# Optimization experiments

Hardware: AMD Instinct MI355X
Metric: run time of the kernel (lower is better)

Reference implementation:

```python
import jax, jax.numpy as jnp
import numpy as np

N = 50000      # nodes
E = 800000     # edges (avg degree 16)
IN = 128       # input feature dim
H = 128        # hidden dim (all layers output H; out_channels unused in source)
DROP_P = 0.5


def setup_inputs() -> dict:
    key = jax.random.key(0)
    ks = jax.random.split(key, 8)
    s_in = 1.0 / np.sqrt(IN).astype(np.float32)
    s_h = 1.0 / np.sqrt(H).astype(np.float32)
    return {
        "x": jax.random.normal(ks[0], (N, IN), jnp.float32),
        "edge_index": jax.random.randint(ks[1], (2, E), 0, N, dtype=jnp.int32),
        "Wl0": jax.random.normal(ks[2], (H, IN), jnp.float32) * s_in,
        "bl0": jnp.zeros((H,), jnp.float32),
        "Wr0": jax.random.normal(ks[3], (H, IN), jnp.float32) * s_in,
        "Wl1": jax.random.normal(ks[4], (H, H), jnp.float32) * s_h,
        "bl1": jnp.zeros((H,), jnp.float32),
        "Wr1": jax.random.normal(ks[5], (H, H), jnp.float32) * s_h,
    }


def _sage_conv(x, src, dst, Wl, bl, Wr):
    # mean-aggregate neighbor messages: gather x[src], scatter-add to dst
    agg = jax.ops.segment_sum(x[src], dst, num_segments=N)          # [N, D]
    deg = jax.ops.segment_sum(jnp.ones((src.shape[0],), x.dtype), dst,
                              num_segments=N)                        # [N]
    agg = agg / jnp.maximum(deg, 1.0)[:, None]                       # scatter_mean (0 for isolated nodes)
    # PyG SAGEConv: lin_l(agg) (with bias) + lin_r(x) (no bias)
    return agg @ Wl.T + bl + x @ Wr.T


def reference(x, edge_index, Wl0, bl0, Wr0, Wl1, bl1, Wr1):
    src, dst = edge_index[0], edge_index[1]
    h = _sage_conv(x, src, dst, Wl0, bl0, Wr0)
    h = jax.nn.relu(h)
    # dropout(p=0.5, training=True) with a fixed key for determinism
    keep = jax.random.bernoulli(jax.random.key(42), 1.0 - DROP_P, h.shape)
    h = jnp.where(keep, h / (1.0 - DROP_P), 0.0)
    out = _sage_conv(h, src, dst, Wl1, bl1, Wr1)
    return out
```

## Files before the change

### kernel.cpp

```cpp
#include <hip/hip_runtime.h>
#include <hip/hip_bf16.h>


#define HDIM 128
#define KDIM 256
#define NBUK 256
#define BNODE 196
#define BCAP 4096
#define BCH 2048

typedef __attribute__((ext_vector_type(8))) short bshort8;
typedef __attribute__((ext_vector_type(4))) float f32x4;
typedef __attribute__((ext_vector_type(2))) float f32x2;

__device__ __forceinline__ ushort f2b(float f) {
  __hip_bfloat16 h = __float2bfloat16(f);
  return *(ushort*)&h;
}
__device__ __forceinline__ unsigned int pack2(float lo, float hi) {
  return (unsigned int)f2b(lo) | ((unsigned int)f2b(hi) << 16);
}

#if __has_builtin(__builtin_amdgcn_cvt_pk_f32_fp8) && __has_builtin(__builtin_amdgcn_cvt_pk_fp8_f32)
#define FP8_HW 1
#endif

__device__ __forceinline__ unsigned int fp8e1(float f) {
  unsigned int u = __float_as_uint(f);
  unsigned int s = (u >> 24) & 0x80u;
  unsigned int mag = u & 0x7FFFFFFFu;
  if (mag < 0x38800000u) return s;
  if (mag > 0x43E00000u) mag = 0x43E00000u;
  unsigned int r = mag + 0x7FFFFu + ((mag >> 20) & 1u);
  return s | ((r >> 20) - 960u);
}
__device__ __forceinline__ float fp8d1(unsigned int b) {
  unsigned int v = b & 0x7Fu;
  float fn = __uint_as_float(((b & 0x80u) << 24) | ((v + 960u) << 20));
  return v >= 8u ? fn : 0.0f;
}

__device__ __forceinline__ unsigned int fp8x4_enc(float f0, float f1, float f2, float f3) {
#ifdef FP8_HW
  int u = 0;
  u = __builtin_amdgcn_cvt_pk_fp8_f32(f0, f1, u, false);
  u = __builtin_amdgcn_cvt_pk_fp8_f32(f2, f3, u, true);
  return (unsigned int)u;
#else
  return fp8e1(f0) | (fp8e1(f1) << 8) | (fp8e1(f2) << 16) | (fp8e1(f3) << 24);
#endif
}
__device__ __forceinline__ void fp8x4_acc(float* a, unsigned int w) {
#ifdef FP8_HW
  f32x2 lo = __builtin_amdgcn_cvt_pk_f32_fp8((int)w, false);
  f32x2 hi = __builtin_amdgcn_cvt_pk_f32_fp8((int)w, true);
  a[0] += lo.x; a[1] += lo.y; a[2] += hi.x; a[3] += hi.y;
#else
  a[0] += fp8d1(w & 255u); a[1] += fp8d1((w >> 8) & 255u);
  a[2] += fp8d1((w >> 16) & 255u); a[3] += fp8d1(w >> 24);
#endif
}

__device__ __forceinline__ unsigned int tf_rotl(unsigned int x, int d) {
  return (x << d) | (x >> (32 - d));
}
__device__ __forceinline__ bool dropout_keep(unsigned int j) {
  unsigned int x0 = 0u, x1 = j;
  const unsigned int ks0 = 0u, ks1 = 42u, ks2 = 0x1BD11BDAu ^ 0u ^ 42u;
  x0 += ks0; x1 += ks1;
#define TF_R(r) { x0 += x1; x1 = tf_rotl(x1, (r)); x1 ^= x0; }
  TF_R(13) TF_R(15) TF_R(26) TF_R(6)
  x0 += ks1; x1 += ks2 + 1u;
  TF_R(17) TF_R(29) TF_R(16) TF_R(24)
  x0 += ks2; x1 += ks0 + 2u;
  TF_R(13) TF_R(15) TF_R(26) TF_R(6)
  x0 += ks0; x1 += ks1 + 3u;
  TF_R(17) TF_R(29) TF_R(16) TF_R(24)
  x0 += ks1; x1 += ks2 + 4u;
  TF_R(13) TF_R(15) TF_R(26) TF_R(6)
  x0 += ks2; x1 += ks0 + 5u;
#undef TF_R
  unsigned int r = x0 ^ x1;
  float u = __uint_as_float((r >> 9) | 0x3f800000u) - 1.0f;
  return u < 0.5f;
}

__global__ __launch_bounds__(256) void bin_cvt_k(
    const int* __restrict__ src, const int* __restrict__ dst,
    int* __restrict__ bucketCount, unsigned int* __restrict__ pairs, int E, int EB,
    const float* __restrict__ x,
    const float* __restrict__ Wl0, const float* __restrict__ Wr0,
    const float* __restrict__ Wl1, const float* __restrict__ Wr1,
    ushort* __restrict__ Xb, unsigned char* __restrict__ Xq,
    ushort* __restrict__ Wc0, ushort* __restrict__ Wc1, int N) {
  __shared__ int hist[NBUK];
  __shared__ int lofs[NBUK];
  __shared__ int lcur[NBUK];
  __shared__ int gbase[NBUK];
  __shared__ unsigned int ordv[BCH];
  __shared__ unsigned char ordb[BCH];

  int b = blockIdx.x;
  if (b >= EB) {
    b -= EB;
    if (b < 64) {
      int t = b * 256 + threadIdx.x;
      int o = t >> 7, k = t & 127;
      Wc0[o * KDIM + k] = f2b(Wl0[t]);
      Wc0[o * KDIM + HDIM + k] = f2b(Wr0[t]);
      Wc1[o * KDIM + k] = f2b(Wl1[t]);
      Wc1[o * KDIM + HDIM + k] = f2b(Wr1[t]);
    } else {
      int t = (b - 64) * 256 + threadIdx.x;
      if (t < N * 32) {
        int n = t >> 5, c4 = t & 31;
        float4 v = *(const float4*)&x[(size_t)n * HDIM + c4 * 4];
        uint2 p;
        p.x = pack2(v.x, v.y);
        p.y = pack2(v.z, v.w);
        *(uint2*)&Xb[(size_t)n * HDIM + c4 * 4] = p;
        *(unsigned int*)&Xq[(size_t)n * HDIM + c4 * 4] = fp8x4_enc(v.x, v.y, v.z, v.w);
      }
    }
    return;
  }

  hist[threadIdx.x] = 0;
  __syncthreads();
  int begin = b * BCH;
  int n = min(BCH, E - begin);
  unsigned int vals[BCH / 256];
  int bks[BCH / 256];
  int cnt = 0;
  for (int i = threadIdx.x; i < n; i += 256) {
    int s = src[begin + i], d = dst[begin + i];
    int bk = d / BNODE;
    int dloc = d - bk * BNODE;
    vals[cnt] = ((unsigned int)s << 8) | (unsigned int)dloc;
    bks[cnt] = bk;
    ++cnt;
    atomicAdd(&hist[bk], 1);
  }
  __syncthreads();
  {
    int v = hist[threadIdx.x];
    lofs[threadIdx.x] = v;
    __syncthreads();
    for (int off = 1; off < NBUK; off <<= 1) {
      int t = (threadIdx.x >= off) ? lofs[threadIdx.x - off] : 0;
      __syncthreads();
      lofs[threadIdx.x] += t;
      __syncthreads();
    }
    int ex = lofs[threadIdx.x] - v;
    __syncthreads();
    lofs[threadIdx.x] = ex;
    lcur[threadIdx.x] = ex;
    gbase[threadIdx.x] = atomicAdd(&bucketCount[threadIdx.x], v);
  }
  __syncthreads();
  for (int k = 0; k < cnt; ++k) {
    int bk = bks[k];
    int p = atomicAdd(&lcur[bk], 1);
    ordv[p] = vals[k];
    ordb[p] = (unsigned char)bk;
  }
  __syncthreads();
  for (int j = threadIdx.x; j < n; j += 256) {
    int bk = ordb[j];
    pairs[bk * BCAP + gbase[bk] + (j - lofs[bk])] = ordv[j];
  }
}

__global__ __launch_bounds__(256) void build_k(const unsigned int* __restrict__ pairs,
                                               const int* __restrict__ bucketCount,
                                               int* __restrict__ deg,
                                               int* __restrict__ rowptr,
                                               ushort* __restrict__ eidx, int N) {
  __shared__ int h[BNODE];
  __shared__ int lofs[BNODE];
  __shared__ int cur[BNODE];
  const int b = blockIdx.x;
  const int base = b * BCAP;
  const int cnt = bucketCount[b];
  const int nodebase = b * BNODE;
  const int nloc = min(BNODE, N - nodebase);
  if (threadIdx.x < BNODE) h[threadIdx.x] = 0;
  __syncthreads();
  for (int i = threadIdx.x; i < cnt; i += 256) atomicAdd(&h[pairs[base + i] & 255u], 1);
  __syncthreads();
  if (threadIdx.x < BNODE) lofs[threadIdx.x] = h[threadIdx.x];
  __syncthreads();
  for (int off = 1; off < BNODE; off <<= 1) {
    int t = (threadIdx.x >= off && threadIdx.x < BNODE) ? lofs[threadIdx.x - off] : 0;
    __syncthreads();
    if (threadIdx.x < BNODE) lofs[threadIdx.x] += t;
    __syncthreads();
  }
  if (threadIdx.x < BNODE) {
    int ex = lofs[threadIdx.x] - h[threadIdx.x];
    cur[threadIdx.x] = ex;
    if (threadIdx.x < nloc) {
      deg[nodebase + threadIdx.x] = h[threadIdx.x];
      rowptr[nodebase + threadIdx.x] = base + ex;
    }
  }
  __syncthreads();
  for (int i = threadIdx.x; i < cnt; i += 256) {
    unsigned int v = pairs[base + i];
    int pos = atomicAdd(&cur[v & 255u], 1);
    eidx[base + pos] = (ushort)(v >> 8);
  }
}

__global__ __launch_bounds__(256) void agg_q(const unsigned char* __restrict__ Fq,
                                             ushort* __restrict__ Ag,
                                             const ushort* __restrict__ eidx,
                                             const int* __restrict__ rowptr,
                                             const int* __restrict__ deg, int N) {
  const int lane = threadIdx.x & 63;
  const int n = blockIdx.x * 4 + (threadIdx.x >> 6);
  if (n >= N) return;
  const int start = rowptr[n];
  const int d = deg[n];
  const int es = lane >> 3;
  const int cl = lane & 7;
  float a[16];
#pragma unroll
  for (int i = 0; i < 16; ++i) a[i] = 0.0f;
  for (int j = 0; j < d; j += 16) {
    uint4 v[2];
    bool m[2];
#pragma unroll
    for (int u = 0; u < 2; ++u) {
      int e = j + u * 8 + es;
      m[u] = e < d;
      if (m[u]) {
        int s = eidx[start + e];
        v[u] = *(const uint4*)&Fq[(size_t)s * HDIM + cl * 16];
      }
    }
#pragma unroll
    for (int u = 0; u < 2; ++u)
      if (m[u]) {
        fp8x4_acc(&a[0], v[u].x);
        fp8x4_acc(&a[4], v[u].y);
        fp8x4_acc(&a[8], v[u].z);
        fp8x4_acc(&a[12], v[u].w);
      }
  }
#pragma unroll
  for (int i = 0; i < 16; ++i) {
    a[i] += __shfl_xor(a[i], 8, 64);
    a[i] += __shfl_xor(a[i], 16, 64);
    a[i] += __shfl_xor(a[i], 32, 64);
  }
  if (es == 0) {
    float rd = 1.0f / fmaxf((float)d, 1.0f);
    uint4 p0, p1;
    p0.x = pack2(a[0] * rd, a[1] * rd);
    p0.y = pack2(a[2] * rd, a[3] * rd);
    p0.z = pack2(a[4] * rd, a[5] * rd);
    p0.w = pack2(a[6] * rd, a[7] * rd);
    p1.x = pack2(a[8] * rd, a[9] * rd);
    p1.y = pack2(a[10] * rd, a[11] * rd);
    p1.z = pack2(a[12] * rd, a[13] * rd);
    p1.w = pack2(a[14] * rd, a[15] * rd);
    *(uint4*)&Ag[(size_t)n * HDIM + cl * 16] = p0;
    *(uint4*)&Ag[(size_t)n * HDIM + cl * 16 + 8] = p1;
  }
}

template <int MODE>
__global__ __launch_bounds__(256) void gemm_mfma(const ushort* __restrict__ Agg,
                                                 const ushort* __restrict__ F,
                                                 const ushort* __restrict__ Wc,
                                                 ushort* __restrict__ hb,
                                                 unsigned char* __restrict__ hq,
                                                 float* __restrict__ fout,
                                                 const float* __restrict__ bias,
                                                 int N) {
  __shared__ char smem[34816];
  ushort* Wl = (ushort*)smem;
  float* Tl = (float*)smem;
  const int tid = threadIdx.x;
  const int lane = tid & 63;
  const int wid = tid >> 6;
  const int quad = lane >> 4;
  const int l15 = lane & 15;
  const int n0 = blockIdx.x * 64;

  int rowA = n0 + wid * 16 + l15;
  if (rowA >= N) rowA = N - 1;
  bshort8 afA[4], afF[4];
#pragma unroll
  for (int ks = 0; ks < 4; ++ks) {
    afA[ks] = *(const bshort8*)&Agg[(size_t)rowA * HDIM + ks * 32 + quad * 8];
    afF[ks] = *(const bshort8*)&F[(size_t)rowA * HDIM + ks * 32 + quad * 8];
  }

  f32x4 acc[8];
#pragma unroll
  for (int i = 0; i < 8; ++i) acc[i] = (f32x4){0.f, 0.f, 0.f, 0.f};

#pragma unroll
  for (int half = 0; half < 2; ++half) {
    __syncthreads();
#pragma unroll
    for (int i = 0; i < 8; ++i) {
      int q = i * 256 + tid;
      int row = q >> 4, seg = q & 15;
      *(uint4*)&Wl[row * 136 + seg * 8] = *(const uint4*)&Wc[row * KDIM + half * HDIM + seg * 8];
    }
    __syncthreads();
#pragma unroll
    for (int ks = 0; ks < 4; ++ks) {
#pragma unroll
      for (int os = 0; os < 8; ++os) {
        bshort8 bf = *(const bshort8*)&Wl[(os * 16 + l15) * 136 + ks * 32 + quad * 8];
        acc[os] = __builtin_amdgcn_mfma_f32_16x16x32_bf16(
            half == 0 ? afA[ks] : afF[ks], bf, acc[os], 0, 0, 0);
      }
    }
  }

  __syncthreads();

  const int wbase = wid * (16 * 132);
#pragma unroll
  for (int os = 0; os < 8; ++os)
#pragma unroll
    for (int r = 0; r < 4; ++r)
      Tl[wbase + (quad * 4 + r) * 132 + os * 16 + l15] = acc[os][r];

  __syncthreads();

#pragma unroll
  for (int i = 0; i < 8; ++i) {
    int q = i * 64 + lane;
    int r = q >> 5;
    int c4 = q & 31;
    int n = n0 + wid * 16 + r;
    if (n >= N) continue;
    int c = c4 * 4;
    float4 v = *(float4*)&Tl[wbase + r * 132 + c];
    const float4 bv = *(const float4*)&bias[c];
    v.x += bv.x; v.y += bv.y; v.z += bv.z; v.w += bv.w;
    if (MODE == 1) {
      v.x = v.x > 0.0f ? v.x : 0.0f;
      v.y = v.y > 0.0f ? v.y : 0.0f;
      v.z = v.z > 0.0f ? v.z : 0.0f;
      v.w = v.w > 0.0f ? v.w : 0.0f;
      unsigned int fj = (unsigned int)n * HDIM + (unsigned int)c;
      v.x = dropout_keep(fj + 0u) ? v.x * 2.0f : 0.0f;
      v.y = dropout_keep(fj + 1u) ? v.y * 2.0f : 0.0f;
      v.z = dropout_keep(fj + 2u) ? v.z * 2.0f : 0.0f;
      v.w = dropout_keep(fj + 3u) ? v.w * 2.0f : 0.0f;
      uint2 p;
      p.x = pack2(v.x, v.y);
      p.y = pack2(v.z, v.w);
      *(uint2*)&hb[(size_t)n * HDIM + c] = p;
      *(unsigned int*)&hq[(size_t)n * HDIM + c] = fp8x4_enc(v.x, v.y, v.z, v.w);
    } else {
      *(float4*)&fout[(size_t)n * HDIM + c] = v;
    }
  }
}

extern "C" void kernel_launch(void* const* d_in, const int* in_sizes, int n_in,
                              void* d_out, int out_size, void* d_ws, size_t ws_size,
                              hipStream_t stream) {
  const float* x   = (const float*)d_in[0];
  const int*   ei  = (const int*)d_in[1];
  const float* Wl0 = (const float*)d_in[2];
  const float* bl0 = (const float*)d_in[3];
  const float* Wr0 = (const float*)d_in[4];
  const float* Wl1 = (const float*)d_in[5];
  const float* bl1 = (const float*)d_in[6];
  const float* Wr1 = (const float*)d_in[7];
  float* out = (float*)d_out;

  const int N = in_sizes[0] / HDIM;
  const int E = in_sizes[1] / 2;
  const int* src = ei;
  const int* dst = ei + E;

  const int Na = (N + 63) & ~63;
  int* bucketCount = (int*)d_ws;
  int* deg         = bucketCount + NBUK;
  int* rowptr      = deg + Na;
  unsigned int* pairs = (unsigned int*)(rowptr + Na);
  ushort* eidx     = (ushort*)(pairs + NBUK * BCAP);
  size_t off = (((size_t)(eidx + NBUK * BCAP) - (size_t)d_ws) + 255) & ~(size_t)255;
  ushort* Wc0 = (ushort*)((char*)d_ws + off);
  ushort* Wc1 = Wc0 + 128 * KDIM;
  ushort* Xb  = Wc1 + 128 * KDIM;
  ushort* Hb  = Xb + (size_t)N * HDIM;
  ushort* Ag  = Hb + (size_t)N * HDIM;
  unsigned char* Xq = (unsigned char*)(Ag + (size_t)N * HDIM);
  unsigned char* Hq = Xq + (size_t)N * HDIM;

  hipMemsetAsync(bucketCount, 0, NBUK * sizeof(int), stream);

  const int EB = (E + BCH - 1) / BCH;
  const int GB = (N + 63) / 64;
  const int AB = (N + 3) / 4;
  const int CB = EB + 64 + (N * 32 + 255) / 256;

  bin_cvt_k<<<CB, 256, 0, stream>>>(src, dst, bucketCount, pairs, E, EB,
                                    x, Wl0, Wr0, Wl1, Wr1, Xb, Xq, Wc0, Wc1, N);
  build_k<<<NBUK, 256, 0, stream>>>(pairs, bucketCount, deg, rowptr, eidx, N);

  agg_q<<<AB, 256, 0, stream>>>(Xq, Ag, eidx, rowptr, deg, N);
  gemm_mfma<1><<<GB, 256, 0, stream>>>(Ag, Xb, Wc0, Hb, Hq, nullptr, bl0, N);
  agg_q<<<AB, 256, 0, stream>>>(Hq, Ag, eidx, rowptr, deg, N);
  gemm_mfma<2><<<GB, 256, 0, stream>>>(Ag, Hb, Wc1, nullptr, nullptr, out, bl1, N);
}
```

Baseline: 210.6 us.

## Slice fp8 feature tables by column and aggregate one slice per block

The fp8 feature tables (Xq, Hq) are re-laid out as 8 column slices of 16 bytes per node, each slice stored contiguously across all nodes. The new aggregation kernel assigns one slice per block, so each gathered slice table (about 800KB) can stay resident in cache, and each wave walks 16 nodes, two at a time, with 4-byte loads. The aim is better cache hit rates for the random neighbor gathers. The cost is narrower loads, more shuffle reductions, per-wave serial node loops, and 8x more edge index reads.

```diff
diff --git a/kernel.cpp b/kernel.cpp
--- a/kernel.cpp
+++ b/kernel.cpp
@@ -119,7 +119,8 @@
         p.x = pack2(v.x, v.y);
         p.y = pack2(v.z, v.w);
         *(uint2*)&Xb[(size_t)n * HDIM + c4 * 4] = p;
-        *(unsigned int*)&Xq[(size_t)n * HDIM + c4 * 4] = fp8x4_enc(v.x, v.y, v.z, v.w);
+        size_t qoff = (size_t)(c4 >> 2) * ((size_t)N * 16) + (size_t)n * 16 + (size_t)(c4 & 3) * 4;
+        *(unsigned int*)&Xq[qoff] = fp8x4_enc(v.x, v.y, v.z, v.w);
       }
     }
     return;
@@ -213,61 +214,69 @@
   }
 }
 
-__global__ __launch_bounds__(256) void agg_q(const unsigned char* __restrict__ Fq,
+__global__ __launch_bounds__(256) void agg_s(const unsigned char* __restrict__ Fq,
                                              ushort* __restrict__ Ag,
                                              const ushort* __restrict__ eidx,
                                              const int* __restrict__ rowptr,
                                              const int* __restrict__ deg, int N) {
+  const int slice = blockIdx.x & 7;
+  const int nb = blockIdx.x >> 3;
   const int lane = threadIdx.x & 63;
-  const int n = blockIdx.x * 4 + (threadIdx.x >> 6);
-  if (n >= N) return;
-  const int start = rowptr[n];
-  const int d = deg[n];
-  const int es = lane >> 3;
-  const int cl = lane & 7;
-  float a[16];
-#pragma unroll
-  for (int i = 0; i < 16; ++i) a[i] = 0.0f;
-  for (int j = 0; j < d; j += 16) {
-    uint4 v[2];
-    bool m[2];
-#pragma unroll
-    for (int u = 0; u < 2; ++u) {
-      int e = j + u * 8 + es;
-      m[u] = e < d;
-      if (m[u]) {
-        int s = eidx[start + e];
-        v[u] = *(const uint4*)&Fq[(size_t)s * HDIM + cl * 16];
+  const int wv = threadIdx.x >> 6;
+  const int es = lane >> 2;
+  const int cl = lane & 3;
+  const unsigned char* Fs = Fq + (size_t)slice * ((size_t)N * 16);
+  const int nbeg = nb * 64 + wv * 16;
+  const int nend = min(nbeg + 16, N);
+  for (int n0 = nbeg; n0 < nend; n0 += 2) {
+    const int n1 = n0 + 1;
+    const bool has1 = n1 < nend;
+    const int r0 = rowptr[n0];
+    const int d0 = deg[n0];
+    const int r1 = has1 ? rowptr[n1] : 0;
+    const int d1 = has1 ? deg[n1] : 0;
+    float a[4] = {0.f, 0.f, 0.f, 0.f};
+    float b[4] = {0.f, 0.f, 0.f, 0.f};
+    const int dm = max(d0, d1);
+    for (int j = 0; j < dm; j += 16) {
+      const int e = j + es;
+      unsigned int w0, w1;
+      const bool m0 = e < d0, m1 = e < d1;
+      if (m0) {
+        int s = eidx[r0 + e];
+        w0 = *(const unsigned int*)&Fs[(size_t)s * 16 + cl * 4];
       }
-    }
-#pragma unroll
-    for (int u = 0; u < 2; ++u)
-      if (m[u]) {
-        fp8x4_acc(&a[0], v[u].x);
-        fp8x4_acc(&a[4], v[u].y);
-        fp8x4_acc(&a[8], v[u].z);
-        fp8x4_acc(&a[12], v[u].w);
+      if (m1) {
+        int s = eidx[r1 + e];
+        w1 = *(const unsigned int*)&Fs[(size_t)s * 16 + cl * 4];
       }
-  }
-#pragma unroll
-  for (int i = 0; i < 16; ++i) {
-    a[i] += __shfl_xor(a[i], 8, 64);
-    a[i] += __shfl_xor(a[i], 16, 64);
-    a[i] += __shfl_xor(a[i], 32, 64);
-  }
-  if (es == 0) {
-    float rd = 1.0f / fmaxf((float)d, 1.0f);
-    uint4 p0, p1;
-    p0.x = pack2(a[0] * rd, a[1] * rd);
-    p0.y = pack2(a[2] * rd, a[3] * rd);
-    p0.z = pack2(a[4] * rd, a[5] * rd);
-    p0.w = pack2(a[6] * rd, a[7] * rd);
-    p1.x = pack2(a[8] * rd, a[9] * rd);
-    p1.y = pack2(a[10] * rd, a[11] * rd);
-    p1.z = pack2(a[12] * rd, a[13] * rd);
-    p1.w = pack2(a[14] * rd, a[15] * rd);
-    *(uint4*)&Ag[(size_t)n * HDIM + cl * 16] = p0;
-    *(uint4*)&Ag[(size_t)n * HDIM + cl * 16 + 8] = p1;
+      if (m0) fp8x4_acc(a, w0);
+      if (m1) fp8x4_acc(b, w1);
+    }
+#pragma unroll
+    for (int i = 0; i < 4; ++i) {
+      a[i] += __shfl_xor(a[i], 4, 64);
+      a[i] += __shfl_xor(a[i], 8, 64);
+      a[i] += __shfl_xor(a[i], 16, 64);
+      a[i] += __shfl_xor(a[i], 32, 64);
+      b[i] += __shfl_xor(b[i], 4, 64);
+      b[i] += __shfl_xor(b[i], 8, 64);
+      b[i] += __shfl_xor(b[i], 16, 64);
+      b[i] += __shfl_xor(b[i], 32, 64);
+    }
+    if (es == 0) {
+      float rd0 = 1.0f / fmaxf((float)d0, 1.0f);
+      uint2 p;
+      p.x = pack2(a[0] * rd0, a[1] * rd0);
+      p.y = pack2(a[2] * rd0, a[3] * rd0);
+      *(uint2*)&Ag[(size_t)n0 * HDIM + slice * 16 + cl * 4] = p;
+      if (has1) {
+        float rd1 = 1.0f / fmaxf((float)d1, 1.0f);
+        p.x = pack2(b[0] * rd1, b[1] * rd1);
+        p.y = pack2(b[2] * rd1, b[3] * rd1);
+        *(uint2*)&Ag[(size_t)n1 * HDIM + slice * 16 + cl * 4] = p;
+      }
+    }
   }
 }
 
@@ -360,7 +369,8 @@
       p.x = pack2(v.x, v.y);
       p.y = pack2(v.z, v.w);
       *(uint2*)&hb[(size_t)n * HDIM + c] = p;
-      *(unsigned int*)&hq[(size_t)n * HDIM + c] = fp8x4_enc(v.x, v.y, v.z, v.w);
+      size_t qoff = (size_t)(c4 >> 2) * ((size_t)N * 16) + (size_t)n * 16 + (size_t)(c & 15);
+      *(unsigned int*)&hq[qoff] = fp8x4_enc(v.x, v.y, v.z, v.w);
     } else {
       *(float4*)&fout[(size_t)n * HDIM + c] = v;
     }
@@ -404,15 +414,15 @@
 
   const int EB = (E + BCH - 1) / BCH;
   const int GB = (N + 63) / 64;
-  const int AB = (N + 3) / 4;
+  const int AS = 8 * ((N + 63) / 64);
   const int CB = EB + 64 + (N * 32 + 255) / 256;
 
   bin_cvt_k<<<CB, 256, 0, stream>>>(src, dst, bucketCount, pairs, E, EB,
                                     x, Wl0, Wr0, Wl1, Wr1, Xb, Xq, Wc0, Wc1, N);
   build_k<<<NBUK, 256, 0, stream>>>(pairs, bucketCount, deg, rowptr, eidx, N);
 
-  agg_q<<<AB, 256, 0, stream>>>(Xq, Ag, eidx, rowptr, deg, N);
+  agg_s<<<AS, 256, 0, stream>>>(Xq, Ag, eidx, rowptr, deg, N);
   gemm_mfma<1><<<GB, 256, 0, stream>>>(Ag, Xb, Wc0, Hb, Hq, nullptr, bl0, N);
-  agg_q<<<AB, 256, 0, stream>>>(Hq, Ag, eidx, rowptr, deg, N);
+  agg_s<<<AS, 256, 0, stream>>>(Hq, Ag, eidx, rowptr, deg, N);
   gemm_mfma<2><<<GB, 256, 0, stream>>>(Ag, Hb, Wc1, nullptr, nullptr, out, bl1, N);
 }
```

Result: slower. 303.5 us (+44.1%).

## Split fp8 feature tables into column halves and aggregate each half separately

Applied to the files above, without the earlier changes.

FP8 features are stored as two planar 64-column halves, and the aggregation kernel launches twice as many blocks, each gathering only one half. The aim is to shrink the randomly gathered working set per pass so neighbor gathers hit cache more often. In exchange, index and degree data are read twice, there are more blocks, and each wave processes more edges with an extra reduction shuffle.

```diff
diff --git a/kernel.cpp b/kernel.cpp
--- a/kernel.cpp
+++ b/kernel.cpp
@@ -119,7 +119,8 @@
         p.x = pack2(v.x, v.y);
         p.y = pack2(v.z, v.w);
         *(uint2*)&Xb[(size_t)n * HDIM + c4 * 4] = p;
-        *(unsigned int*)&Xq[(size_t)n * HDIM + c4 * 4] = fp8x4_enc(v.x, v.y, v.z, v.w);
+        size_t qoff = (size_t)(c4 >> 4) * ((size_t)N * 64) + (size_t)n * 64 + (size_t)(c4 & 15) * 4;
+        *(unsigned int*)&Xq[qoff] = fp8x4_enc(v.x, v.y, v.z, v.w);
       }
     }
     return;
@@ -213,31 +214,35 @@
   }
 }
 
-__global__ __launch_bounds__(256) void agg_q(const unsigned char* __restrict__ Fq,
+__global__ __launch_bounds__(256) void agg_h(const unsigned char* __restrict__ Fq,
                                              ushort* __restrict__ Ag,
                                              const ushort* __restrict__ eidx,
                                              const int* __restrict__ rowptr,
-                                             const int* __restrict__ deg, int N) {
+                                             const int* __restrict__ deg, int N, int NB) {
+  int b = blockIdx.x;
+  const int half = (b >= NB) ? 1 : 0;
+  b -= half * NB;
   const int lane = threadIdx.x & 63;
-  const int n = blockIdx.x * 4 + (threadIdx.x >> 6);
+  const int n = b * 4 + (threadIdx.x >> 6);
   if (n >= N) return;
+  const unsigned char* Fs = Fq + (size_t)half * ((size_t)N * 64);
   const int start = rowptr[n];
   const int d = deg[n];
-  const int es = lane >> 3;
-  const int cl = lane & 7;
+  const int es = lane >> 2;
+  const int cl = lane & 3;
   float a[16];
 #pragma unroll
   for (int i = 0; i < 16; ++i) a[i] = 0.0f;
-  for (int j = 0; j < d; j += 16) {
+  for (int j = 0; j < d; j += 32) {
     uint4 v[2];
     bool m[2];
 #pragma unroll
     for (int u = 0; u < 2; ++u) {
-      int e = j + u * 8 + es;
+      int e = j + u * 16 + es;
       m[u] = e < d;
       if (m[u]) {
         int s = eidx[start + e];
-        v[u] = *(const uint4*)&Fq[(size_t)s * HDIM + cl * 16];
+        v[u] = *(const uint4*)&Fs[(size_t)s * 64 + cl * 16];
       }
     }
 #pragma unroll
@@ -251,6 +256,7 @@
   }
 #pragma unroll
   for (int i = 0; i < 16; ++i) {
+    a[i] += __shfl_xor(a[i], 4, 64);
     a[i] += __shfl_xor(a[i], 8, 64);
     a[i] += __shfl_xor(a[i], 16, 64);
     a[i] += __shfl_xor(a[i], 32, 64);
@@ -266,8 +272,9 @@
     p1.y = pack2(a[10] * rd, a[11] * rd);
     p1.z = pack2(a[12] * rd, a[13] * rd);
     p1.w = pack2(a[14] * rd, a[15] * rd);
-    *(uint4*)&Ag[(size_t)n * HDIM + cl * 16] = p0;
-    *(uint4*)&Ag[(size_t)n * HDIM + cl * 16 + 8] = p1;
+    ushort* dstp = &Ag[(size_t)n * HDIM + half * 64 + cl * 16];
+    *(uint4*)dstp = p0;
+    *(uint4*)(dstp + 8) = p1;
   }
 }
 
@@ -360,7 +367,8 @@
       p.x = pack2(v.x, v.y);
       p.y = pack2(v.z, v.w);
       *(uint2*)&hb[(size_t)n * HDIM + c] = p;
-      *(unsigned int*)&hq[(size_t)n * HDIM + c] = fp8x4_enc(v.x, v.y, v.z, v.w);
+      size_t qoff = (size_t)(c4 >> 4) * ((size_t)N * 64) + (size_t)n * 64 + (size_t)(c4 & 15) * 4;
+      *(unsigned int*)&hq[qoff] = fp8x4_enc(v.x, v.y, v.z, v.w);
     } else {
       *(float4*)&fout[(size_t)n * HDIM + c] = v;
     }
@@ -404,15 +412,15 @@
 
   const int EB = (E + BCH - 1) / BCH;
   const int GB = (N + 63) / 64;
-  const int AB = (N + 3) / 4;
+  const int NB = (N + 3) / 4;
   const int CB = EB + 64 + (N * 32 + 255) / 256;
 
   bin_cvt_k<<<CB, 256, 0, stream>>>(src, dst, bucketCount, pairs, E, EB,
                                     x, Wl0, Wr0, Wl1, Wr1, Xb, Xq, Wc0, Wc1, N);
   build_k<<<NBUK, 256, 0, stream>>>(pairs, bucketCount, deg, rowptr, eidx, N);
 
-  agg_q<<<AB, 256, 0, stream>>>(Xq, Ag, eidx, rowptr, deg, N);
+  agg_h<<<2 * NB, 256, 0, stream>>>(Xq, Ag, eidx, rowptr, deg, N, NB);
   gemm_mfma<1><<<GB, 256, 0, stream>>>(Ag, Xb, Wc0, Hb, Hq, nullptr, bl0, N);
-  agg_q<<<AB, 256, 0, stream>>>(Hq, Ag, eidx, rowptr, deg, N);
+  agg_h<<<2 * NB, 256, 0, stream>>>(Hq, Ag, eidx, rowptr, deg, N, NB);
   gemm_mfma<2><<<GB, 256, 0, stream>>>(Ag, Hb, Wc1, nullptr, nullptr, out, bl1, N);
 }
```

Measured after the change: 287.5 us. 36.5% more time.

## Fuse all stages into one cooperative persistent kernel with grid syncs

Applied to the files above, without the earlier changes.

Replaces the memset and six separate kernel launches with a single cooperative persistent kernel. Each stage runs as a grid-stride loop over virtual blocks, with grid.sync between stages, and a multi-launch fallback is kept in case the cooperative launch fails. The goal is to remove launch gaps and inter-kernel drain and refill. The change also swaps the padded LDS layouts in the GEMM for XOR and rotation swizzles, cutting LDS to 32KB to fit more blocks per CU. The costs are grid-barrier overhead, lower occupancy from launch bounds and the large shared buffer, and poorer load balance within a persistent grid.

```diff
diff --git a/kernel.cpp b/kernel.cpp
--- a/kernel.cpp
+++ b/kernel.cpp
@@ -1,5 +1,8 @@
 #include <hip/hip_runtime.h>
 #include <hip/hip_bf16.h>
+#include <hip/hip_cooperative_groups.h>
+
+namespace cg = cooperative_groups;
 
 
 #define HDIM 128
@@ -12,6 +15,20 @@
 typedef __attribute__((ext_vector_type(8))) short bshort8;
 typedef __attribute__((ext_vector_type(4))) float f32x4;
 typedef __attribute__((ext_vector_type(2))) float f32x2;
+
+struct MegaArgs {
+  const int* src; const int* dst;
+  int* bucketCount; unsigned int* pairs;
+  int* deg; int* rowptr; ushort* eidx;
+  const float* x;
+  const float* Wl0; const float* bl0; const float* Wr0;
+  const float* Wl1; const float* bl1; const float* Wr1;
+  ushort* Xb; ushort* Hb; ushort* Ag;
+  unsigned char* Xq; unsigned char* Hq;
+  ushort* Wc0; ushort* Wc1;
+  float* out;
+  int E, EB, CB, GB, AB, N;
+};
 
 __device__ __forceinline__ ushort f2b(float f) {
   __hip_bfloat16 h = __float2bfloat16(f);
@@ -85,41 +102,34 @@
   return u < 0.5f;
 }
 
-__global__ __launch_bounds__(256) void bin_cvt_k(
-    const int* __restrict__ src, const int* __restrict__ dst,
-    int* __restrict__ bucketCount, unsigned int* __restrict__ pairs, int E, int EB,
-    const float* __restrict__ x,
-    const float* __restrict__ Wl0, const float* __restrict__ Wr0,
-    const float* __restrict__ Wl1, const float* __restrict__ Wr1,
-    ushort* __restrict__ Xb, unsigned char* __restrict__ Xq,
-    ushort* __restrict__ Wc0, ushort* __restrict__ Wc1, int N) {
-  __shared__ int hist[NBUK];
-  __shared__ int lofs[NBUK];
-  __shared__ int lcur[NBUK];
-  __shared__ int gbase[NBUK];
-  __shared__ unsigned int ordv[BCH];
-  __shared__ unsigned char ordb[BCH];
-
-  int b = blockIdx.x;
-  if (b >= EB) {
-    b -= EB;
+
+__device__ __forceinline__ void bin_cvt_body(const MegaArgs& A, int b, char* smem) {
+  int* hist = (int*)smem;
+  int* lofs = hist + NBUK;
+  int* lcur = lofs + NBUK;
+  int* gbase = lcur + NBUK;
+  unsigned int* ordv = (unsigned int*)(gbase + NBUK);
+  unsigned char* ordb = (unsigned char*)(ordv + BCH);
+
+  if (b >= A.EB) {
+    b -= A.EB;
     if (b < 64) {
       int t = b * 256 + threadIdx.x;
       int o = t >> 7, k = t & 127;
-      Wc0[o * KDIM + k] = f2b(Wl0[t]);
-      Wc0[o * KDIM + HDIM + k] = f2b(Wr0[t]);
-      Wc1[o * KDIM + k] = f2b(Wl1[t]);
-      Wc1[o * KDIM + HDIM + k] = f2b(Wr1[t]);
+      A.Wc0[o * KDIM + k] = f2b(A.Wl0[t]);
+      A.Wc0[o * KDIM + HDIM + k] = f2b(A.Wr0[t]);
+      A.Wc1[o * KDIM + k] = f2b(A.Wl1[t]);
+      A.Wc1[o * KDIM + HDIM + k] = f2b(A.Wr1[t]);
     } else {
       int t = (b - 64) * 256 + threadIdx.x;
-      if (t < N * 32) {
+      if (t < A.N * 32) {
         int n = t >> 5, c4 = t & 31;
-        float4 v = *(const float4*)&x[(size_t)n * HDIM + c4 * 4];
+        float4 v = *(const float4*)&A.x[(size_t)n * HDIM + c4 * 4];
         uint2 p;
         p.x = pack2(v.x, v.y);
         p.y = pack2(v.z, v.w);
-        *(uint2*)&Xb[(size_t)n * HDIM + c4 * 4] = p;
-        *(unsigned int*)&Xq[(size_t)n * HDIM + c4 * 4] = fp8x4_enc(v.x, v.y, v.z, v.w);
+        *(uint2*)&A.Xb[(size_t)n * HDIM + c4 * 4] = p;
+        *(unsigned int*)&A.Xq[(size_t)n * HDIM + c4 * 4] = fp8x4_enc(v.x, v.y, v.z, v.w);
       }
     }
     return;
@@ -128,12 +138,12 @@
   hist[threadIdx.x] = 0;
   __syncthreads();
   int begin = b * BCH;
-  int n = min(BCH, E - begin);
+  int n = min(BCH, A.E - begin);
   unsigned int vals[BCH / 256];
   int bks[BCH / 256];
   int cnt = 0;
   for (int i = threadIdx.x; i < n; i += 256) {
-    int s = src[begin + i], d = dst[begin + i];
+    int s = A.src[begin + i], d = A.dst[begin + i];
     int bk = d / BNODE;
     int dloc = d - bk * BNODE;
     vals[cnt] = ((unsigned int)s << 8) | (unsigned int)dloc;
@@ -156,7 +166,7 @@
     __syncthreads();
     lofs[threadIdx.x] = ex;
     lcur[threadIdx.x] = ex;
-    gbase[threadIdx.x] = atomicAdd(&bucketCount[threadIdx.x], v);
+    gbase[threadIdx.x] = atomicAdd(&A.bucketCount[threadIdx.x], v);
   }
   __syncthreads();
   for (int k = 0; k < cnt; ++k) {
@@ -168,26 +178,21 @@
   __syncthreads();
   for (int j = threadIdx.x; j < n; j += 256) {
     int bk = ordb[j];
-    pairs[bk * BCAP + gbase[bk] + (j - lofs[bk])] = ordv[j];
-  }
-}
-
-__global__ __launch_bounds__(256) void build_k(const unsigned int* __restrict__ pairs,
-                                               const int* __restrict__ bucketCount,
-                                               int* __restrict__ deg,
-                                               int* __restrict__ rowptr,
-                                               ushort* __restrict__ eidx, int N) {
-  __shared__ int h[BNODE];
-  __shared__ int lofs[BNODE];
-  __shared__ int cur[BNODE];
-  const int b = blockIdx.x;
+    A.pairs[bk * BCAP + gbase[bk] + (j - lofs[bk])] = ordv[j];
+  }
+}
+
+__device__ __forceinline__ void build_body(const MegaArgs& A, int b, char* smem) {
+  int* h = (int*)smem;
+  int* lofs = h + BNODE;
+  int* cur = lofs + BNODE;
   const int base = b * BCAP;
-  const int cnt = bucketCount[b];
+  const int cnt = A.bucketCount[b];
   const int nodebase = b * BNODE;
-  const int nloc = min(BNODE, N - nodebase);
+  const int nloc = min(BNODE, A.N - nodebase);
   if (threadIdx.x < BNODE) h[threadIdx.x] = 0;
   __syncthreads();
-  for (int i = threadIdx.x; i < cnt; i += 256) atomicAdd(&h[pairs[base + i] & 255u], 1);
+  for (int i = threadIdx.x; i < cnt; i += 256) atomicAdd(&h[A.pairs[base + i] & 255u], 1);
   __syncthreads();
   if (threadIdx.x < BNODE) lofs[threadIdx.x] = h[threadIdx.x];
   __syncthreads();
@@ -201,25 +206,25 @@
     int ex = lofs[threadIdx.x] - h[threadIdx.x];
     cur[threadIdx.x] = ex;
     if (threadIdx.x < nloc) {
-      deg[nodebase + threadIdx.x] = h[threadIdx.x];
-      rowptr[nodebase + threadIdx.x] = base + ex;
+      A.deg[nodebase + threadIdx.x] = h[threadIdx.x];
+      A.rowptr[nodebase + threadIdx.x] = base + ex;
     }
   }
   __syncthreads();
   for (int i = threadIdx.x; i < cnt; i += 256) {
-    unsigned int v = pairs[base + i];
+    unsigned int v = A.pairs[base + i];
     int pos = atomicAdd(&cur[v & 255u], 1);
-    eidx[base + pos] = (ushort)(v >> 8);
-  }
-}
-
-__global__ __launch_bounds__(256) void agg_q(const unsigned char* __restrict__ Fq,
-                                             ushort* __restrict__ Ag,
-                                             const ushort* __restrict__ eidx,
-                                             const int* __restrict__ rowptr,
-                                             const int* __restrict__ deg, int N) {
+    A.eidx[base + pos] = (ushort)(v >> 8);
+  }
+}
+
+__device__ __forceinline__ void agg_body(const unsigned char* __restrict__ Fq,
+                                         ushort* __restrict__ Ag,
+                                         const ushort* __restrict__ eidx,
+                                         const int* __restrict__ rowptr,
+                                         const int* __restrict__ deg, int N, int vb) {
   const int lane = threadIdx.x & 63;
-  const int n = blockIdx.x * 4 + (threadIdx.x >> 6);
+  const int n = vb * 4 + (threadIdx.x >> 6);
   if (n >= N) return;
   const int start = rowptr[n];
   const int d = deg[n];
@@ -271,24 +276,20 @@
   }
 }
 
-template <int MODE>
-__global__ __launch_bounds__(256) void gemm_mfma(const ushort* __restrict__ Agg,
-                                                 const ushort* __restrict__ F,
-                                                 const ushort* __restrict__ Wc,
-                                                 ushort* __restrict__ hb,
-                                                 unsigned char* __restrict__ hq,
-                                                 float* __restrict__ fout,
-                                                 const float* __restrict__ bias,
-                                                 int N) {
-  __shared__ char smem[34816];
+__device__ __forceinline__ void gemm_body(const MegaArgs& A, int vb, int mode, char* smem) {
   ushort* Wl = (ushort*)smem;
   float* Tl = (float*)smem;
+  const ushort* Agg = A.Ag;
+  const ushort* F = (mode == 1) ? A.Xb : A.Hb;
+  const ushort* Wc = (mode == 1) ? A.Wc0 : A.Wc1;
+  const float* bias = (mode == 1) ? A.bl0 : A.bl1;
+  const int N = A.N;
   const int tid = threadIdx.x;
   const int lane = tid & 63;
   const int wid = tid >> 6;
   const int quad = lane >> 4;
   const int l15 = lane & 15;
-  const int n0 = blockIdx.x * 64;
+  const int n0 = vb * 64;
 
   int rowA = n0 + wid * 16 + l15;
   if (rowA >= N) rowA = N - 1;
@@ -309,15 +310,16 @@
 #pragma unroll
     for (int i = 0; i < 8; ++i) {
       int q = i * 256 + tid;
-      int row = q >> 4, seg = q & 15;
-      *(uint4*)&Wl[row * 136 + seg * 8] = *(const uint4*)&Wc[row * KDIM + half * HDIM + seg * 8];
+      int row = q >> 4, u = q & 15;
+      *(uint4*)&Wl[row * 128 + ((u ^ (row & 15)) << 3)] =
+          *(const uint4*)&Wc[row * KDIM + half * HDIM + u * 8];
     }
     __syncthreads();
 #pragma unroll
     for (int ks = 0; ks < 4; ++ks) {
 #pragma unroll
       for (int os = 0; os < 8; ++os) {
-        bshort8 bf = *(const bshort8*)&Wl[(os * 16 + l15) * 136 + ks * 32 + quad * 8];
+        bshort8 bf = *(const bshort8*)&Wl[(os * 16 + l15) * 128 + (((ks * 4 + quad) ^ l15) << 3)];
         acc[os] = __builtin_amdgcn_mfma_f32_16x16x32_bf16(
             half == 0 ? afA[ks] : afF[ks], bf, acc[os], 0, 0, 0);
       }
@@ -326,12 +328,14 @@
 
   __syncthreads();
 
-  const int wbase = wid * (16 * 132);
+  const int wbase = wid * (16 * 128);
 #pragma unroll
   for (int os = 0; os < 8; ++os)
 #pragma unroll
-    for (int r = 0; r < 4; ++r)
-      Tl[wbase + (quad * 4 + r) * 132 + os * 16 + l15] = acc[os][r];
+    for (int r = 0; r < 4; ++r) {
+      int row = quad * 4 + r;
+      Tl[wbase + row * 128 + ((os * 16 + l15 + 4 * row) & 127)] = acc[os][r];
+    }
 
   __syncthreads();
 
@@ -343,10 +347,10 @@
     int n = n0 + wid * 16 + r;
     if (n >= N) continue;
     int c = c4 * 4;
-    float4 v = *(float4*)&Tl[wbase + r * 132 + c];
+    float4 v = *(float4*)&Tl[wbase + r * 128 + ((c + 4 * r) & 127)];
     const float4 bv = *(const float4*)&bias[c];
     v.x += bv.x; v.y += bv.y; v.z += bv.z; v.w += bv.w;
-    if (MODE == 1) {
+    if (mode == 1) {
       v.x = v.x > 0.0f ? v.x : 0.0f;
       v.y = v.y > 0.0f ? v.y : 0.0f;
       v.z = v.z > 0.0f ? v.z : 0.0f;
@@ -359,60 +363,117 @@
       uint2 p;
       p.x = pack2(v.x, v.y);
       p.y = pack2(v.z, v.w);
-      *(uint2*)&hb[(size_t)n * HDIM + c] = p;
-      *(unsigned int*)&hq[(size_t)n * HDIM + c] = fp8x4_enc(v.x, v.y, v.z, v.w);
+      *(uint2*)&A.Hb[(size_t)n * HDIM + c] = p;
+      *(unsigned int*)&A.Hq[(size_t)n * HDIM + c] = fp8x4_enc(v.x, v.y, v.z, v.w);
     } else {
-      *(float4*)&fout[(size_t)n * HDIM + c] = v;
-    }
-  }
+      *(float4*)&A.out[(size_t)n * HDIM + c] = v;
+    }
+  }
+}
+
+__global__ __launch_bounds__(256, 5) void mega_k(MegaArgs A) {
+  cg::grid_group grid = cg::this_grid();
+  __shared__ char smem[32768];
+  const int gb = gridDim.x;
+
+  if (blockIdx.x == 0 && threadIdx.x < NBUK) A.bucketCount[threadIdx.x] = 0;
+  grid.sync();
+  for (int vb = blockIdx.x; vb < A.CB; vb += gb) { bin_cvt_body(A, vb, smem); __syncthreads(); }
+  grid.sync();
+  for (int vb = blockIdx.x; vb < NBUK; vb += gb) { build_body(A, vb, smem); __syncthreads(); }
+  grid.sync();
+  for (int vb = blockIdx.x; vb < A.AB; vb += gb)
+    agg_body(A.Xq, A.Ag, A.eidx, A.rowptr, A.deg, A.N, vb);
+  grid.sync();
+  for (int vb = blockIdx.x; vb < A.GB; vb += gb) { gemm_body(A, vb, 1, smem); __syncthreads(); }
+  grid.sync();
+  for (int vb = blockIdx.x; vb < A.AB; vb += gb)
+    agg_body(A.Hq, A.Ag, A.eidx, A.rowptr, A.deg, A.N, vb);
+  grid.sync();
+  for (int vb = blockIdx.x; vb < A.GB; vb += gb) { gemm_body(A, vb, 2, smem); __syncthreads(); }
+}
+
+__global__ __launch_bounds__(256) void w_bin(MegaArgs A) {
+  __shared__ char s[16384];
+  bin_cvt_body(A, blockIdx.x, s);
+}
+__global__ __launch_bounds__(256) void w_build(MegaArgs A) {
+  __shared__ char s[2368];
+  build_body(A, blockIdx.x, s);
+}
+__global__ __launch_bounds__(256) void w_agg(MegaArgs A, int layer) {
+  agg_body(layer == 1 ? A.Xq : A.Hq, A.Ag, A.eidx, A.rowptr, A.deg, A.N, blockIdx.x);
+}
+__global__ __launch_bounds__(256) void w_gemm(MegaArgs A, int mode) {
+  __shared__ char s[32768];
+  gemm_body(A, blockIdx.x, mode, s);
 }
 
 extern "C" void kernel_launch(void* const* d_in, const int* in_sizes, int n_in,
                               void* d_out, int out_size, void* d_ws, size_t ws_size,
                               hipStream_t stream) {
-  const float* x   = (const float*)d_in[0];
-  const int*   ei  = (const int*)d_in[1];
-  const float* Wl0 = (const float*)d_in[2];
-  const float* bl0 = (const float*)d_in[3];
-  const float* Wr0 = (const float*)d_in[4];
-  const float* Wl1 = (const float*)d_in[5];
-  const float* bl1 = (const float*)d_in[6];
-  const float* Wr1 = (const float*)d_in[7];
-  float* out = (float*)d_out;
-
   const int N = in_sizes[0] / HDIM;
   const int E = in_sizes[1] / 2;
-  const int* src = ei;
-  const int* dst = ei + E;
+
+  MegaArgs A;
+  A.x   = (const float*)d_in[0];
+  const int* ei = (const int*)d_in[1];
+  A.Wl0 = (const float*)d_in[2];
+  A.bl0 = (const float*)d_in[3];
+  A.Wr0 = (const float*)d_in[4];
+  A.Wl1 = (const float*)d_in[5];
+  A.bl1 = (const float*)d_in[6];
+  A.Wr1 = (const float*)d_in[7];
+  A.out = (float*)d_out;
+  A.src = ei;
+  A.dst = ei + E;
+  A.E = E;
+  A.N = N;
 
   const int Na = (N + 63) & ~63;
-  int* bucketCount = (int*)d_ws;
-  int* deg         = bucketCount + NBUK;
-  int* rowptr      = deg + Na;
-  unsigned int* pairs = (unsigned int*)(rowptr + Na);
-  ushort* eidx     = (ushort*)(pairs + NBUK * BCAP);
-  size_t off = (((size_t)(eidx + NBUK * BCAP) - (size_t)d_ws) + 255) & ~(size_t)255;
-  ushort* Wc0 = (ushort*)((char*)d_ws + off);
-  ushort* Wc1 = Wc0 + 128 * KDIM;
-  ushort* Xb  = Wc1 + 128 * KDIM;
-  ushort* Hb  = Xb + (size_t)N * HDIM;
-  ushort* Ag  = Hb + (size_t)N * HDIM;
-  unsigned char* Xq = (unsigned char*)(Ag + (size_t)N * HDIM);
-  unsigned char* Hq = Xq + (size_t)N * HDIM;
-
-  hipMemsetAsync(bucketCount, 0, NBUK * sizeof(int), stream);
-
-  const int EB = (E + BCH - 1) / BCH;
-  const int GB = (N + 63) / 64;
-  const int AB = (N + 3) / 4;
-  const int CB = EB + 64 + (N * 32 + 255) / 256;
-
-  bin_cvt_k<<<CB, 256, 0, stream>>>(src, dst, bucketCount, pairs, E, EB,
-                                    x, Wl0, Wr0, Wl1, Wr1, Xb, Xq, Wc0, Wc1, N);
-  build_k<<<NBUK, 256, 0, stream>>>(pairs, bucketCount, deg, rowptr, eidx, N);
-
-  agg_q<<<AB, 256, 0, stream>>>(Xq, Ag, eidx, rowptr, deg, N);
-  gemm_mfma<1><<<GB, 256, 0, stream>>>(Ag, Xb, Wc0, Hb, Hq, nullptr, bl0, N);
-  agg_q<<<AB, 256, 0, stream>>>(Hq, Ag, eidx, rowptr, deg, N);
-  gemm_mfma<2><<<GB, 256, 0, stream>>>(Ag, Hb, Wc1, nullptr, nullptr, out, bl1, N);
-}
+  A.bucketCount = (int*)d_ws;
+  A.deg         = A.bucketCount + NBUK;
+  A.rowptr      = A.deg + Na;
+  A.pairs       = (unsigned int*)(A.rowptr + Na);
+  A.eidx        = (ushort*)(A.pairs + NBUK * BCAP);
+  size_t off = (((size_t)(A.eidx + NBUK * BCAP) - (size_t)d_ws) + 255) & ~(size_t)255;
+  A.Wc0 = (ushort*)((char*)d_ws + off);
+  A.Wc1 = A.Wc0 + 128 * KDIM;
+  A.Xb  = A.Wc1 + 128 * KDIM;
+  A.Hb  = A.Xb + (size_t)N * HDIM;
+  A.Ag  = A.Hb + (size_t)N * HDIM;
+  A.Xq  = (unsigned char*)(A.Ag + (size_t)N * HDIM);
+  A.Hq  = A.Xq + (size_t)N * HDIM;
+
+  A.EB = (E + BCH - 1) / BCH;
+  A.GB = (N + 63) / 64;
+  A.AB = (N + 3) / 4;
+  A.CB = A.EB + 64 + (N * 32 + 255) / 256;
+
+  static int grid_blocks = 0;
+  if (grid_blocks == 0) {
+    int dev = 0;
+    hipGetDevice(&dev);
+    int nb = 0;
+    hipOccupancyMaxActiveBlocksPerMultiprocessor(&nb, mega_k, 256, 0);
+    if (nb < 1) nb = 1;
+    int cus = 0;
+    hipDeviceGetAttribute(&cus, hipDeviceAttributeMultiprocessorCount, dev);
+    if (cus < 1) cus = 256;
+    grid_blocks = nb * cus;
+  }
+
+  void* kargs[1] = {(void*)&A};
+  hipError_t err = hipLaunchCooperativeKernel((const void*)mega_k, dim3(grid_blocks),
+                                              dim3(256), kargs, 0, stream);
+  if (err != hipSuccess) {
+    (void)hipGetLastError();
+    hipMemsetAsync(A.bucketCount, 0, NBUK * sizeof(int), stream);
+    w_bin<<<A.CB, 256, 0, stream>>>(A);
+    w_build<<<NBUK, 256, 0, stream>>>(A);
+    w_agg<<<A.AB, 256, 0, stream>>>(A, 1);
+    w_gemm<<<A.GB, 256, 0, stream>>>(A, 1);
+    w_agg<<<A.AB, 256, 0, stream>>>(A, 2);
+    w_gemm<<<A.GB, 256, 0, stream>>>(A, 2);
+  }
+}
```

Result: slower. 695.5 us (+230.3%).
